# Kernel optimization log

Hardware: AMD Instinct MI355X
Metric: run time of the kernel (lower is better)

Reference implementation:

```python
import jax, jax.numpy as jnp
import numpy as np
from jax import lax

B, D = 8192, 1024
N_STEPS = 50
LR, B1, B2, EPS = 0.01, 0.9, 0.999, 1e-8  # torch.optim.Adam defaults except lr


def setup_inputs() -> dict:
    key = jax.random.key(0)
    k1, k2, k3 = jax.random.split(key, 3)
    s = jax.random.normal(k1, (B, D), jnp.float32)
    target_confidence = jax.random.uniform(k2, (B, 1), jnp.float32)
    # nn.Linear(style_dim, 1) params
    W = jax.random.normal(k3, (1, D), jnp.float32) * (1.0 / np.sqrt(D))
    b = jnp.zeros((1,), jnp.float32)
    return {"s": s, "target_confidence": target_confidence, "W": W, "b": b}


def reference(s, target_confidence, W, b):
    # Analytic gradient of total_loss = mean((sigmoid(sp@W.T+b)-t)^2) + mean(|sp - s|)
    # w.r.t. sp. sign(0)=0 matches torch's grad of |x| at 0.
    n_mse = float(B * 1)   # prediction has B*1 elements
    n_l1 = float(B * D)
    def grad_loss(sp):
        p = jax.nn.sigmoid(sp @ W.T + b)                  # [B,1]
        g_z = (2.0 / n_mse) * (p - target_confidence) * p * (1.0 - p)  # dL/dz
        g = g_z @ W                                       # [B,D]
        return g + jnp.sign(sp - s) / n_l1

    def adam_step(carry, t):
        sp, m, v = carry
        g = grad_loss(sp)
        m = B1 * m + (1.0 - B1) * g
        v = B2 * v + (1.0 - B2) * g * g
        m_hat = m / (1.0 - B1 ** t)
        v_hat = v / (1.0 - B2 ** t)
        sp = sp - LR * m_hat / (jnp.sqrt(v_hat) + EPS)
        return (sp, m, v), None

    zeros = jnp.zeros_like(s)
    ts = jnp.arange(1, N_STEPS + 1, dtype=s.dtype)  # Adam step counter starts at 1
    (sp, _, _), _ = lax.scan(adam_step, (s, zeros, zeros), ts)
    return sp
```

## Files before the change

kernel.cpp:

```cpp
#include <hip/hip_runtime.h>
#include <math.h>

#define NROWS   8192
#define DDIM    1024
#define NSTEPS  50
#define NPAIR   8
#define WPB     4

#define LR_D   0.01
#define B1_D   0.9
#define B2_D   0.999
#define EPS_D  1e-8

typedef __attribute__((ext_vector_type(2))) float f32x2;

struct StepTbl {
    float alpha[NSTEPS];
    float eps2[NSTEPS];
    float delta[NSTEPS];
};

template <int CTRL>
__device__ __forceinline__ float dppf(float v) {
    return __builtin_bit_cast(float,
        __builtin_amdgcn_update_dpp(0, __builtin_bit_cast(int, v), CTRL, 0xF, 0xF, true));
}

__device__ __forceinline__ float wave_sum(float v) {
    v += dppf<0xB1>(v);
    v += dppf<0x4E>(v);
    v += dppf<0x124>(v);
    v += dppf<0x128>(v);
    v += __shfl_xor(v, 16, 64);
    v += __shfl_xor(v, 32, 64);
    return v;
}

__device__ __forceinline__ float sign_bfi(float d, unsigned smask, float smag) {
    float r;
    asm("v_bfi_b32 %0, %1, %2, %3" : "=v"(r) : "v"(smask), "v"(d), "v"(smag));
    return r;
}

__global__ __launch_bounds__(256) void adam_rows_kernel(
    const float* __restrict__ s,
    const float* __restrict__ tconf,
    const float* __restrict__ W,
    const float* __restrict__ bias,
    float* __restrict__ out,
    const StepTbl tbl)
{
    const int lane = threadIdx.x & 63;
    const int wave = threadIdx.x >> 6;
    const int row  = blockIdx.x * WPB + wave;

    const float bb = bias[0];
    const float tc = tconf[row];

    const float GZS      = 2.0f / (float)NROWS;
    const float NLOG2E   = -1.44269504f;
    const unsigned SMASK = 0x80000000u;
    const float    SMAG  = 1.1920929e-7f;

    const f32x2 b12  = {0.9f, 0.9f};
    const f32x2 b22  = {0.999f, 0.999f};
    const f32x2 two2 = {2.0f, 2.0f};

    f32x2 w2[NPAIR], diff2[NPAIR], M2[NPAIR], V2[NPAIR];

    const float4* W4 = reinterpret_cast<const float4*>(W);
    const float4* S4 = reinterpret_cast<const float4*>(s + (size_t)row * DDIM);

    float dot0 = 0.0f;
    #pragma unroll
    for (int c = 0; c < 4; ++c) {
        float4 wv = W4[c * 64 + lane];
        float4 sv = S4[c * 64 + lane];
        w2[2*c+0] = (f32x2){wv.x, wv.y};
        w2[2*c+1] = (f32x2){wv.z, wv.w};
        dot0 = fmaf(sv.x, wv.x, dot0);
        dot0 = fmaf(sv.y, wv.y, dot0);
        dot0 = fmaf(sv.z, wv.z, dot0);
        dot0 = fmaf(sv.w, wv.w, dot0);
    }
    const float zb = wave_sum(dot0) + bb;

    float ddot = 0.0f;

    {
        const float e  = __builtin_amdgcn_exp2f(zb * NLOG2E);
        const float p  = __builtin_amdgcn_rcpf(1.0f + e);
        const float gz = GZS * (p - tc) * (p * (1.0f - p));

        const f32x2 gz2  = {gz, gz};
        const f32x2 nal2 = {-tbl.alpha[0], -tbl.alpha[0]};
        const f32x2 ep2  = {tbl.eps2[0], tbl.eps2[0]};
        const f32x2 de2  = {tbl.delta[0], tbl.delta[0]};

        #pragma unroll
        for (int i = 0; i < NPAIR; ++i) {
            const f32x2 g = gz2 * w2[i];
            M2[i] = g;
            V2[i] = g * g;

            const f32x2 vd = V2[i] + de2;
            f32x2 u;
            u.x = __builtin_amdgcn_rsqf(vd.x);
            u.y = __builtin_amdgcn_rsqf(vd.y);

            const f32x2 den = __builtin_elementwise_fma(V2[i], u, ep2);
            const f32x2 e2  = __builtin_elementwise_fma(-den, u, two2);
            const f32x2 r   = u * e2;
            const f32x2 q   = M2[i] * r;

            diff2[i] = nal2 * q;

            ddot = fmaf(diff2[i].x, w2[i].x, ddot);
            ddot = fmaf(diff2[i].y, w2[i].y, ddot);
        }
    }

    for (int step = 1; step < NSTEPS; ++step) {
        const float z  = zb + wave_sum(ddot);
        const float e  = __builtin_amdgcn_exp2f(z * NLOG2E);
        const float p  = __builtin_amdgcn_rcpf(1.0f + e);
        const float gz = GZS * (p - tc) * (p * (1.0f - p));

        const float alpha = tbl.alpha[step];
        const float eps2  = tbl.eps2[step];
        const float delta = tbl.delta[step];

        const f32x2 gz2  = {gz, gz};
        const f32x2 nal2 = {-alpha, -alpha};
        const f32x2 ep2  = {eps2, eps2};
        const f32x2 de2  = {delta, delta};

        ddot = 0.0f;
        #pragma unroll
        for (int i = 0; i < NPAIR; ++i) {
            f32x2 sg;
            sg.x = sign_bfi(diff2[i].x, SMASK, SMAG);
            sg.y = sign_bfi(diff2[i].y, SMASK, SMAG);

            const f32x2 g = __builtin_elementwise_fma(gz2, w2[i], sg);

            M2[i] = __builtin_elementwise_fma(b12, M2[i], g);
            V2[i] = __builtin_elementwise_fma(g, g, V2[i] * b22);

            const f32x2 vd = V2[i] + de2;
            f32x2 u;
            u.x = __builtin_amdgcn_rsqf(vd.x);
            u.y = __builtin_amdgcn_rsqf(vd.y);

            const f32x2 den = __builtin_elementwise_fma(V2[i], u, ep2);
            const f32x2 e2  = __builtin_elementwise_fma(-den, u, two2);
            const f32x2 r   = u * e2;
            const f32x2 q   = M2[i] * r;

            diff2[i] = __builtin_elementwise_fma(nal2, q, diff2[i]);

            ddot = fmaf(diff2[i].x, w2[i].x, ddot);
            ddot = fmaf(diff2[i].y, w2[i].y, ddot);
        }
    }

    float4* O4 = reinterpret_cast<float4*>(out + (size_t)row * DDIM);
    #pragma unroll
    for (int c = 0; c < 4; ++c) {
        float4 sv = S4[c * 64 + lane];
        float4 ov;
        ov.x = sv.x + diff2[2*c+0].x;
        ov.y = sv.y + diff2[2*c+0].y;
        ov.z = sv.z + diff2[2*c+1].x;
        ov.w = sv.w + diff2[2*c+1].y;
        O4[c * 64 + lane] = ov;
    }
}

extern "C" void kernel_launch(void* const* d_in, const int* in_sizes, int n_in,
                              void* d_out, int out_size, void* d_ws, size_t ws_size,
                              hipStream_t stream) {
    const float* s     = (const float*)d_in[0];
    const float* tconf = (const float*)d_in[1];
    const float* W     = (const float*)d_in[2];
    const float* bias  = (const float*)d_in[3];
    float* out = (float*)d_out;

    StepTbl tbl;
    double b1p = 1.0, b2p = 1.0;
    for (int t = 0; t < NSTEPS; ++t) {
        b1p *= B1_D;
        b2p *= B2_D;
        const double c1 = 1.0 - b1p;
        const double c2 = 1.0 - b2p;
        const double sc = sqrt(c2 / (1.0 - B2_D));
        tbl.alpha[t] = (float)(LR_D * (1.0 - B1_D) * sc / c1);
        tbl.eps2[t]  = (float)(EPS_D * sc);
        tbl.delta[t] = tbl.eps2[t] * tbl.eps2[t];
    }

    dim3 grid(NROWS / WPB);
    dim3 block(64 * WPB);
    adam_rows_kernel<<<grid, block, 0, stream>>>(s, tconf, W, bias, out, tbl);
}
```

Baseline: 123.7 us.

## Process two interleaved rows per wave with persistent grid of 512 blocks

```diff
diff --git a/kernel.cpp b/kernel.cpp
--- a/kernel.cpp
+++ b/kernel.cpp
@@ -6,6 +6,9 @@
 #define NSTEPS  50
 #define NPAIR   8
 #define WPB     4
+#define NBLOCKS 512
+#define TOTWAVES (NBLOCKS * WPB)
+#define RPWAVE  2
 
 #define LR_D   0.01
 #define B1_D   0.9
@@ -52,10 +55,9 @@
 {
     const int lane = threadIdx.x & 63;
     const int wave = threadIdx.x >> 6;
-    const int row  = blockIdx.x * WPB + wave;
+    const int wi   = blockIdx.x * WPB + wave;
 
     const float bb = bias[0];
-    const float tc = tconf[row];
 
     const float GZS      = 2.0f / (float)NROWS;
     const float NLOG2E   = -1.44269504f;
@@ -66,114 +68,174 @@
     const f32x2 b22  = {0.999f, 0.999f};
     const f32x2 two2 = {2.0f, 2.0f};
 
-    f32x2 w2[NPAIR], diff2[NPAIR], M2[NPAIR], V2[NPAIR];
-
+    f32x2 w2[NPAIR];
     const float4* W4 = reinterpret_cast<const float4*>(W);
-    const float4* S4 = reinterpret_cast<const float4*>(s + (size_t)row * DDIM);
-
-    float dot0 = 0.0f;
     #pragma unroll
     for (int c = 0; c < 4; ++c) {
         float4 wv = W4[c * 64 + lane];
-        float4 sv = S4[c * 64 + lane];
         w2[2*c+0] = (f32x2){wv.x, wv.y};
         w2[2*c+1] = (f32x2){wv.z, wv.w};
-        dot0 = fmaf(sv.x, wv.x, dot0);
-        dot0 = fmaf(sv.y, wv.y, dot0);
-        dot0 = fmaf(sv.z, wv.z, dot0);
-        dot0 = fmaf(sv.w, wv.w, dot0);
     }
-    const float zb = wave_sum(dot0) + bb;
-
-    float ddot = 0.0f;
-
-    {
-        const float e  = __builtin_amdgcn_exp2f(zb * NLOG2E);
-        const float p  = __builtin_amdgcn_rcpf(1.0f + e);
-        const float gz = GZS * (p - tc) * (p * (1.0f - p));
-
-        const f32x2 gz2  = {gz, gz};
-        const f32x2 nal2 = {-tbl.alpha[0], -tbl.alpha[0]};
-        const f32x2 ep2  = {tbl.eps2[0], tbl.eps2[0]};
-        const f32x2 de2  = {tbl.delta[0], tbl.delta[0]};
-
+
+    for (int rp = 0; rp < RPWAVE; ++rp) {
+        const int rowA = 2 * (wi + rp * TOTWAVES);
+        const int rowB = rowA + 1;
+
+        const float tcA = tconf[rowA];
+        const float tcB = tconf[rowB];
+
+        const float4* SA4 = reinterpret_cast<const float4*>(s + (size_t)rowA * DDIM);
+        const float4* SB4 = reinterpret_cast<const float4*>(s + (size_t)rowB * DDIM);
+
+        float dotA = 0.0f, dotB = 0.0f;
         #pragma unroll
-        for (int i = 0; i < NPAIR; ++i) {
-            const f32x2 g = gz2 * w2[i];
-            M2[i] = g;
-            V2[i] = g * g;
-
-            const f32x2 vd = V2[i] + de2;
-            f32x2 u;
-            u.x = __builtin_amdgcn_rsqf(vd.x);
-            u.y = __builtin_amdgcn_rsqf(vd.y);
-
-            const f32x2 den = __builtin_elementwise_fma(V2[i], u, ep2);
-            const f32x2 e2  = __builtin_elementwise_fma(-den, u, two2);
-            const f32x2 r   = u * e2;
-            const f32x2 q   = M2[i] * r;
-
-            diff2[i] = nal2 * q;
-
-            ddot = fmaf(diff2[i].x, w2[i].x, ddot);
-            ddot = fmaf(diff2[i].y, w2[i].y, ddot);
-        }
-    }
-
-    for (int step = 1; step < NSTEPS; ++step) {
-        const float z  = zb + wave_sum(ddot);
-        const float e  = __builtin_amdgcn_exp2f(z * NLOG2E);
-        const float p  = __builtin_amdgcn_rcpf(1.0f + e);
-        const float gz = GZS * (p - tc) * (p * (1.0f - p));
-
-        const float alpha = tbl.alpha[step];
-        const float eps2  = tbl.eps2[step];
-        const float delta = tbl.delta[step];
-
-        const f32x2 gz2  = {gz, gz};
-        const f32x2 nal2 = {-alpha, -alpha};
-        const f32x2 ep2  = {eps2, eps2};
-        const f32x2 de2  = {delta, delta};
-
-        ddot = 0.0f;
+        for (int c = 0; c < 4; ++c) {
+            float4 sa = SA4[c * 64 + lane];
+            float4 sb = SB4[c * 64 + lane];
+            dotA = fmaf(sa.x, w2[2*c+0].x, dotA);
+            dotA = fmaf(sa.y, w2[2*c+0].y, dotA);
+            dotA = fmaf(sa.z, w2[2*c+1].x, dotA);
+            dotA = fmaf(sa.w, w2[2*c+1].y, dotA);
+            dotB = fmaf(sb.x, w2[2*c+0].x, dotB);
+            dotB = fmaf(sb.y, w2[2*c+0].y, dotB);
+            dotB = fmaf(sb.z, w2[2*c+1].x, dotB);
+            dotB = fmaf(sb.w, w2[2*c+1].y, dotB);
+        }
+        const float zbA = wave_sum(dotA) + bb;
+        const float zbB = wave_sum(dotB) + bb;
+
+        f32x2 dA[NPAIR], MA[NPAIR], VA[NPAIR];
+        f32x2 dB[NPAIR], MB[NPAIR], VB[NPAIR];
+
+        float ddA = 0.0f, ddB = 0.0f;
+
+        {
+            const float eA  = __builtin_amdgcn_exp2f(zbA * NLOG2E);
+            const float pA  = __builtin_amdgcn_rcpf(1.0f + eA);
+            const float gzA = GZS * (pA - tcA) * (pA * (1.0f - pA));
+            const float eB  = __builtin_amdgcn_exp2f(zbB * NLOG2E);
+            const float pB  = __builtin_amdgcn_rcpf(1.0f + eB);
+            const float gzB = GZS * (pB - tcB) * (pB * (1.0f - pB));
+
+            const f32x2 gzA2 = {gzA, gzA};
+            const f32x2 gzB2 = {gzB, gzB};
+            const f32x2 nal2 = {-tbl.alpha[0], -tbl.alpha[0]};
+            const f32x2 ep2  = {tbl.eps2[0], tbl.eps2[0]};
+            const f32x2 de2  = {tbl.delta[0], tbl.delta[0]};
+
+            #pragma unroll
+            for (int i = 0; i < NPAIR; ++i) {
+                {
+                    const f32x2 g = gzA2 * w2[i];
+                    MA[i] = g;  VA[i] = g * g;
+                    const f32x2 vd = VA[i] + de2;
+                    f32x2 u;
+                    u.x = __builtin_amdgcn_rsqf(vd.x);
+                    u.y = __builtin_amdgcn_rsqf(vd.y);
+                    const f32x2 den = __builtin_elementwise_fma(VA[i], u, ep2);
+                    const f32x2 e2  = __builtin_elementwise_fma(-den, u, two2);
+                    const f32x2 r   = u * e2;
+                    dA[i] = nal2 * (MA[i] * r);
+                    ddA = fmaf(dA[i].x, w2[i].x, ddA);
+                    ddA = fmaf(dA[i].y, w2[i].y, ddA);
+                }
+                {
+                    const f32x2 g = gzB2 * w2[i];
+                    MB[i] = g;  VB[i] = g * g;
+                    const f32x2 vd = VB[i] + de2;
+                    f32x2 u;
+                    u.x = __builtin_amdgcn_rsqf(vd.x);
+                    u.y = __builtin_amdgcn_rsqf(vd.y);
+                    const f32x2 den = __builtin_elementwise_fma(VB[i], u, ep2);
+                    const f32x2 e2  = __builtin_elementwise_fma(-den, u, two2);
+                    const f32x2 r   = u * e2;
+                    dB[i] = nal2 * (MB[i] * r);
+                    ddB = fmaf(dB[i].x, w2[i].x, ddB);
+                    ddB = fmaf(dB[i].y, w2[i].y, ddB);
+                }
+            }
+        }
+
+        for (int step = 1; step < NSTEPS; ++step) {
+            const float zA  = zbA + wave_sum(ddA);
+            const float zB  = zbB + wave_sum(ddB);
+            const float eA  = __builtin_amdgcn_exp2f(zA * NLOG2E);
+            const float pA  = __builtin_amdgcn_rcpf(1.0f + eA);
+            const float gzA = GZS * (pA - tcA) * (pA * (1.0f - pA));
+            const float eB  = __builtin_amdgcn_exp2f(zB * NLOG2E);
+            const float pB  = __builtin_amdgcn_rcpf(1.0f + eB);
+            const float gzB = GZS * (pB - tcB) * (pB * (1.0f - pB));
+
+            const float alpha = tbl.alpha[step];
+            const float eps2  = tbl.eps2[step];
+            const float delta = tbl.delta[step];
+
+            const f32x2 gzA2 = {gzA, gzA};
+            const f32x2 gzB2 = {gzB, gzB};
+            const f32x2 nal2 = {-alpha, -alpha};
+            const f32x2 ep2  = {eps2, eps2};
+            const f32x2 de2  = {delta, delta};
+
+            ddA = 0.0f; ddB = 0.0f;
+            #pragma unroll
+            for (int i = 0; i < NPAIR; ++i) {
+                {
+                    f32x2 sg;
+                    sg.x = sign_bfi(dA[i].x, SMASK, SMAG);
+                    sg.y = sign_bfi(dA[i].y, SMASK, SMAG);
+                    const f32x2 g = __builtin_elementwise_fma(gzA2, w2[i], sg);
+                    MA[i] = __builtin_elementwise_fma(b12, MA[i], g);
+                    VA[i] = __builtin_elementwise_fma(g, g, VA[i] * b22);
+                    const f32x2 vd = VA[i] + de2;
+                    f32x2 u;
+                    u.x = __builtin_amdgcn_rsqf(vd.x);
+                    u.y = __builtin_amdgcn_rsqf(vd.y);
+                    const f32x2 den = __builtin_elementwise_fma(VA[i], u, ep2);
+                    const f32x2 e2  = __builtin_elementwise_fma(-den, u, two2);
+                    const f32x2 r   = u * e2;
+                    dA[i] = __builtin_elementwise_fma(nal2, MA[i] * r, dA[i]);
+                    ddA = fmaf(dA[i].x, w2[i].x, ddA);
+                    ddA = fmaf(dA[i].y, w2[i].y, ddA);
+                }
+                {
+                    f32x2 sg;
+                    sg.x = sign_bfi(dB[i].x, SMASK, SMAG);
+                    sg.y = sign_bfi(dB[i].y, SMASK, SMAG);
+                    const f32x2 g = __builtin_elementwise_fma(gzB2, w2[i], sg);
+                    MB[i] = __builtin_elementwise_fma(b12, MB[i], g);
+                    VB[i] = __builtin_elementwise_fma(g, g, VB[i] * b22);
+                    const f32x2 vd = VB[i] + de2;
+                    f32x2 u;
+                    u.x = __builtin_amdgcn_rsqf(vd.x);
+                    u.y = __builtin_amdgcn_rsqf(vd.y);
+                    const f32x2 den = __builtin_elementwise_fma(VB[i], u, ep2);
+                    const f32x2 e2  = __builtin_elementwise_fma(-den, u, two2);
+                    const f32x2 r   = u * e2;
+                    dB[i] = __builtin_elementwise_fma(nal2, MB[i] * r, dB[i]);
+                    ddB = fmaf(dB[i].x, w2[i].x, ddB);
+                    ddB = fmaf(dB[i].y, w2[i].y, ddB);
+                }
+            }
+        }
+
+        float4* OA4 = reinterpret_cast<float4*>(out + (size_t)rowA * DDIM);
+        float4* OB4 = reinterpret_cast<float4*>(out + (size_t)rowB * DDIM);
         #pragma unroll
-        for (int i = 0; i < NPAIR; ++i) {
-            f32x2 sg;
-            sg.x = sign_bfi(diff2[i].x, SMASK, SMAG);
-            sg.y = sign_bfi(diff2[i].y, SMASK, SMAG);
-
-            const f32x2 g = __builtin_elementwise_fma(gz2, w2[i], sg);
-
-            M2[i] = __builtin_elementwise_fma(b12, M2[i], g);
-            V2[i] = __builtin_elementwise_fma(g, g, V2[i] * b22);
-
-            const f32x2 vd = V2[i] + de2;
-            f32x2 u;
-            u.x = __builtin_amdgcn_rsqf(vd.x);
-            u.y = __builtin_amdgcn_rsqf(vd.y);
-
-            const f32x2 den = __builtin_elementwise_fma(V2[i], u, ep2);
-            const f32x2 e2  = __builtin_elementwise_fma(-den, u, two2);
-            const f32x2 r   = u * e2;
-            const f32x2 q   = M2[i] * r;
-
-            diff2[i] = __builtin_elementwise_fma(nal2, q, diff2[i]);
-
-            ddot = fmaf(diff2[i].x, w2[i].x, ddot);
-            ddot = fmaf(diff2[i].y, w2[i].y, ddot);
-        }
-    }
-
-    float4* O4 = reinterpret_cast<float4*>(out + (size_t)row * DDIM);
-    #pragma unroll
-    for (int c = 0; c < 4; ++c) {
-        float4 sv = S4[c * 64 + lane];
-        float4 ov;
-        ov.x = sv.x + diff2[2*c+0].x;
-        ov.y = sv.y + diff2[2*c+0].y;
-        ov.z = sv.z + diff2[2*c+1].x;
-        ov.w = sv.w + diff2[2*c+1].y;
-        O4[c * 64 + lane] = ov;
+        for (int c = 0; c < 4; ++c) {
+            float4 sa = SA4[c * 64 + lane];
+            float4 sb = SB4[c * 64 + lane];
+            float4 oa, ob;
+            oa.x = sa.x + dA[2*c+0].x;
+            oa.y = sa.y + dA[2*c+0].y;
+            oa.z = sa.z + dA[2*c+1].x;
+            oa.w = sa.w + dA[2*c+1].y;
+            ob.x = sb.x + dB[2*c+0].x;
+            ob.y = sb.y + dB[2*c+0].y;
+            ob.z = sb.z + dB[2*c+1].x;
+            ob.w = sb.w + dB[2*c+1].y;
+            OA4[c * 64 + lane] = oa;
+            OB4[c * 64 + lane] = ob;
+        }
     }
 }
 
@@ -199,7 +261,7 @@
         tbl.delta[t] = tbl.eps2[t] * tbl.eps2[t];
     }
 
-    dim3 grid(NROWS / WPB);
+    dim3 grid(NBLOCKS);
     dim3 block(64 * WPB);
     adam_rows_kernel<<<grid, block, 0, stream>>>(s, tconf, W, bias, out, tbl);
 }
```

After: 138.0 us. 1.12x slower.
